# Performance work log

Hardware: AMD Instinct MI355X
Metric: run time of the kernel (lower is better)

Reference implementation:

```python
import jax, jax.numpy as jnp
import numpy as np

K = 9          # kernel_size
PAD = 4        # padding
N_OUT, C_IN = 32, 32


def setup_inputs() -> dict:
    key = jax.random.key(0)
    k1, k2, k3, k4, k5 = jax.random.split(key, 5)
    x = jax.random.normal(k1, (16, C_IN, 192, 192), jnp.float32)
    sx = jax.random.uniform(k2, (N_OUT, C_IN), jnp.float32, 0.2, 4.0)
    sy = jax.random.uniform(k3, (N_OUT, C_IN), jnp.float32, 0.2, 4.0)
    th = jax.random.uniform(k4, (N_OUT, C_IN), jnp.float32, 0.0, 2.0 * np.pi)
    weight = jnp.stack([sx, sy, th], axis=-1)          # [N, C, 3]
    bias = jax.random.normal(k5, (N_OUT,), jnp.float32) * 0.01
    return {"x": x, "weight": weight, "bias": bias}


def _gaussian_kernels(weight, k):
    # weight: [N, C, 3] -> normalized anisotropic Gaussian kernels [N, C, k, k]
    sx, sy = weight[..., 0], weight[..., 1]
    rad = weight[..., 2] / 180.0 * jnp.pi          # matches theta/180*pi in source
    c, s = jnp.cos(rad), jnp.sin(rad)
    sx2, sy2 = sx * sx, sy * sy
    # Sigma = U diag(sx^2, sy^2) U^T, U = [[c,-s],[s,c]] -> Sigma = [[a,b],[b,d]]
    a = c * c * sx2 + s * s * sy2
    b = c * s * (sx2 - sy2)
    d = s * s * sx2 + c * c * sy2
    det = a * d - b * b
    ia, ib, id_ = d / det, -b / det, a / det       # closed-form 2x2 inverse
    ax = jnp.arange(k, dtype=jnp.float32) - k // 2
    xx = ax[None, :]                               # x varies along columns
    yy = ax[:, None]                               # y varies along rows
    # quadratic form: ia*x^2 + 2*ib*x*y + id*y^2, broadcast to [N, C, k, k]
    q = (ia[..., None, None] * (xx * xx)
         + 2.0 * ib[..., None, None] * (xx * yy)
         + id_[..., None, None] * (yy * yy))
    ker = jnp.exp(-0.5 * q)
    return ker / jnp.sum(ker, axis=(-2, -1), keepdims=True)


def reference(x, weight, bias):
    w = _gaussian_kernels(weight, K)               # [N, C, K, K]
    out = jax.lax.conv_general_dilated(
        x, w, window_strides=(1, 1), padding=[(PAD, PAD), (PAD, PAD)],
        dimension_numbers=("NCHW", "OIHW", "NCHW"))
    return out + bias[None, :, None, None]
```

## Files before the change

kernel.cpp:

```cpp
#include <hip/hip_runtime.h>
#include <stdint.h>

#define H 192
#define W 192
#define CIN 32
#define NOUT 32
#define NB 16
#define PADI 4
#define HP 200
#define WP 200

#define HT 16
#define WTL 16
#define RROWS 24
#define RCOLS 24

typedef __attribute__((ext_vector_type(8))) short bf16x8;
typedef __attribute__((ext_vector_type(4))) float f32x4;

__device__ __forceinline__ unsigned short f2bf(float f) {
    union { float f; unsigned int u; } v; v.f = f;
    unsigned int r = v.u + 0x7fffu + ((v.u >> 16) & 1u);
    return (unsigned short)(r >> 16);
}

__device__ __forceinline__ void gload_lds16(const void* g, void* l) {
    __builtin_amdgcn_global_load_lds(
        (const __attribute__((address_space(1))) void*)g,
        (__attribute__((address_space(3))) void*)l, 16, 0, 0);
}

__global__ void genw_kernel(const float* __restrict__ wp, unsigned short* __restrict__ W2g) {
    const int b = blockIdx.x;
    const int o = b >> 5;
    const int i = b & 31;
    const int t = threadIdx.x;

    float sx = wp[b * 3 + 0], sy = wp[b * 3 + 1], th = wp[b * 3 + 2];
    float rad = th / 180.0f * 3.14159265358979323846f;
    float co = cosf(rad), si = sinf(rad);
    float sx2 = sx * sx, sy2 = sy * sy;
    float a = co * co * sx2 + si * si * sy2;
    float bb = co * si * (sx2 - sy2);
    float d = si * si * sx2 + co * co * sy2;
    float det = a * d - bb * bb;
    float ia = d / det, ib = -bb / det, idd = a / det;

    const int tap = t;
    float e = 0.0f;
    if (tap < 81) {
        float xx = (float)(tap % 9 - 4);
        float yy = (float)(tap / 9 - 4);
        float q = ia * xx * xx + 2.0f * ib * xx * yy + idd * yy * yy;
        e = expf(-0.5f * q);
    }
    float s = e;
    #pragma unroll
    for (int off = 32; off > 0; off >>= 1) s += __shfl_down(s, off);
    __shared__ float ws[2];
    if ((t & 63) == 0) ws[t >> 6] = s;
    __syncthreads();
    float total = ws[0] + ws[1];

    if (tap < 81) {
        int mt = o >> 4, m = o & 15, quad = i >> 3, j = i & 7;
        W2g[((((mt * 81 + tap) * 4 + quad) * 16 + m) << 3) + j] = f2bf(e / total);
    }
}

__global__ __launch_bounds__(256) void xpad_kernel(
    const float* __restrict__ x, unsigned short* __restrict__ xb)
{
    const int gid = blockIdx.x * 256 + threadIdx.x;
    const int wp4 = gid % (WP / 4);
    int rest = gid / (WP / 4);
    const int rp = rest % HP;
    rest /= HP;
    const int quad = rest & 3;
    const int n = rest >> 2;

    const int row = rp - PADI;
    const int col0 = wp4 * 4 - PADI;

    unsigned int d[4][4];
    #pragma unroll
    for (int p = 0; p < 4; p++)
        #pragma unroll
        for (int j = 0; j < 4; j++) d[p][j] = 0u;

    if ((unsigned)row < (unsigned)H && col0 >= 0 && col0 <= W - 4) {
        const float* p0 = x + (((size_t)(n * CIN + quad * 8)) * H + row) * (size_t)W + col0;
        #pragma unroll
        for (int k = 0; k < 8; ++k) {
            float4 v = *(const float4*)(p0 + (size_t)k * H * W);
            const int j = k >> 1;
            const int sh = (k & 1) * 16;
            d[0][j] |= (unsigned int)f2bf(v.x) << sh;
            d[1][j] |= (unsigned int)f2bf(v.y) << sh;
            d[2][j] |= (unsigned int)f2bf(v.z) << sh;
            d[3][j] |= (unsigned int)f2bf(v.w) << sh;
        }
    }
    unsigned short* dst = xb + (size_t)gid * 32;
    #pragma unroll
    for (int p = 0; p < 4; p++)
        *(uint4*)(dst + p * 8) = make_uint4(d[p][0], d[p][1], d[p][2], d[p][3]);
}

__global__ __launch_bounds__(512, 6) void conv_kernel(
    const unsigned short* __restrict__ xb, const unsigned short* __restrict__ W2g,
    const float* __restrict__ bias, float* __restrict__ out)
{
    __shared__ __align__(16) unsigned short ldsx[4 * RROWS * RCOLS * 8];

    const int t = threadIdx.x;
    const int bid = (blockIdx.x & 7) * 288 + (blockIdx.x >> 3);
    const int wb = bid % (W / WTL);
    const int hb = (bid / (W / WTL)) % (H / HT);
    const int n  = bid / ((W / WTL) * (H / HT));
    const int r0p = hb * HT;
    const int c0p = wb * WTL;
    const unsigned short* xbn = xb + (size_t)n * 4 * HP * WP * 8;

    #pragma unroll
    for (int it = 0; it < 4; ++it) {
        const int idx = it * 512 + t;
        const int w = idx % RCOLS;
        const int r = (idx / RCOLS) % RROWS;
        const int quad = idx / (RCOLS * RROWS);
        const size_t goff = (((size_t)(quad * HP + r0p + r)) * WP + (c0p + w)) * 8;
        gload_lds16(xbn + goff, &ldsx[(size_t)idx * 8]);
    }
    if (t < 256) {
        const int idx = 2048 + t;
        const int w = idx % RCOLS;
        const int r = (idx / RCOLS) % RROWS;
        const int quad = idx / (RCOLS * RROWS);
        const size_t goff = (((size_t)(quad * HP + r0p + r)) * WP + (c0p + w)) * 8;
        gload_lds16(xbn + goff, &ldsx[(size_t)idx * 8]);
    }

    const int wave = t >> 6;
    const int lane = t & 63;
    const int l15 = lane & 15;
    const int quad4 = lane >> 4;
    const int mt = wave & 1;
    const int rbase = (wave >> 1) * 4;

    const bf16x8* __restrict__ wbase =
        (const bf16x8*)W2g + (mt * 81 * 64 + quad4 * 16 + l15);

    bf16x8 A[9];
    #pragma unroll
    for (int dy = 0; dy < 9; dy++)
        A[dy] = wbase[(dy * 9 + 0) * 64];

    __syncthreads();

    f32x4 acc[4];
    #pragma unroll
    for (int i = 0; i < 4; i++) acc[i] = (f32x4){0.f, 0.f, 0.f, 0.f};

    const unsigned short* bptr = &ldsx[(size_t)(((quad4 * RROWS + rbase) * RCOLS) + l15) * 8];

    for (int dx = 0; dx < 9; dx++) {
        if (dx) {
            #pragma unroll
            for (int dy = 0; dy < 9; dy++)
                A[dy] = wbase[(dy * 9 + dx) * 64];
        }
        __builtin_amdgcn_s_setprio(1);
        bf16x8 bcur = *(const bf16x8*)&bptr[(size_t)(0 * RCOLS + dx) * 8];
        #pragma unroll
        for (int rr = 0; rr < 12; rr++) {
            const bf16x8 bnxt = (rr < 11)
                ? *(const bf16x8*)&bptr[(size_t)((rr + 1) * RCOLS + dx) * 8]
                : bcur;
            #pragma unroll
            for (int dy = 0; dy < 9; dy++) {
                const int orr = rr - dy;
                if (orr >= 0 && orr < 4) {
                    acc[orr] = __builtin_amdgcn_mfma_f32_16x16x32_bf16(
                        A[dy], bcur, acc[orr], 0, 0, 0);
                }
            }
            bcur = bnxt;
        }
        __builtin_amdgcn_s_setprio(0);
    }

    float* outn = out + (size_t)n * NOUT * H * W;
    float bb[4];
    #pragma unroll
    for (int reg = 0; reg < 4; reg++) bb[reg] = bias[mt * 16 + quad4 * 4 + reg];
    #pragma unroll
    for (int orr = 0; orr < 4; orr++) {
        const int row = hb * HT + rbase + orr;
        const int col = wb * WTL + l15;
        #pragma unroll
        for (int reg = 0; reg < 4; reg++) {
            const int och = mt * 16 + quad4 * 4 + reg;
            outn[((size_t)och * H + row) * W + col] = acc[orr][reg] + bb[reg];
        }
    }
}

__global__ __launch_bounds__(256, 4) void conv_kernel_legacy(
    const float* __restrict__ x, const unsigned short* __restrict__ W2g,
    const float* __restrict__ bias, float* __restrict__ out)
{
    __shared__ __align__(16) unsigned short ldsx[4 * RROWS * RCOLS * 8];

    const int t = threadIdx.x;
    const int bid = (blockIdx.x & 7) * 288 + (blockIdx.x >> 3);
    const int wb = bid % (W / WTL);
    const int hb = (bid / (W / WTL)) % (H / HT);
    const int n  = bid / ((W / WTL) * (H / HT));
    const int row0 = hb * HT - PADI;
    const int col0 = wb * WTL - PADI;
    const float* xn = x + (size_t)n * CIN * H * W;

    float v[9][8];
    #pragma unroll
    for (int it = 0; it < 9; ++it) {
        int idx = it * 256 + t;
        int w = idx % RCOLS;
        int r = (idx / RCOLS) % RROWS;
        int quad = idx / (RCOLS * RROWS);
        int row = row0 + r, col = col0 + w;
        #pragma unroll
        for (int k = 0; k < 8; k++) v[it][k] = 0.0f;
        if ((unsigned)row < (unsigned)H && (unsigned)col < (unsigned)W) {
            const float* p = xn + ((size_t)(quad * 8) * H + row) * W + col;
            #pragma unroll
            for (int k = 0; k < 8; k++) v[it][k] = p[(size_t)k * H * W];
        }
    }
    #pragma unroll
    for (int it = 0; it < 9; ++it) {
        int idx = it * 256 + t;
        unsigned int d[4];
        #pragma unroll
        for (int k = 0; k < 4; k++)
            d[k] = (unsigned int)f2bf(v[it][2 * k]) | ((unsigned int)f2bf(v[it][2 * k + 1]) << 16);
        *(uint4*)&ldsx[(size_t)idx * 8] = make_uint4(d[0], d[1], d[2], d[3]);
    }

    const int wave = t >> 6;
    const int lane = t & 63;
    const int l15 = lane & 15;
    const int quad4 = lane >> 4;
    const int mt = wave & 1;
    const int rbase = (wave >> 1) * 8;

    const bf16x8* __restrict__ Wpt = (const bf16x8*)W2g;

    bf16x8 A[2][9];
    #pragma unroll
    for (int dy = 0; dy < 9; dy++)
        A[0][dy] = Wpt[((mt * 81 + dy * 9 + 0) * 4 + quad4) * 16 + l15];

    __syncthreads();

    f32x4 acc[8];
    #pragma unroll
    for (int i = 0; i < 8; i++) acc[i] = (f32x4){0.f, 0.f, 0.f, 0.f};

    const unsigned short* bptr = &ldsx[(size_t)(((quad4 * RROWS + rbase) * RCOLS) + l15) * 8];

    #pragma unroll
    for (int dx = 0; dx < 9; dx++) {
        const int cur = dx & 1, nxt = cur ^ 1;
        if (dx < 8) {
            #pragma unroll
            for (int dy = 0; dy < 9; dy++)
                A[nxt][dy] = Wpt[((mt * 81 + dy * 9 + (dx + 1)) * 4 + quad4) * 16 + l15];
        }
        #pragma unroll
        for (int rr = 0; rr < 16; rr++) {
            const bf16x8 bfrag = *(const bf16x8*)&bptr[(size_t)(rr * RCOLS + dx) * 8];
            #pragma unroll
            for (int dy = 0; dy < 9; dy++) {
                const int orr = rr - dy;
                if (orr >= 0 && orr < 8) {
                    acc[orr] = __builtin_amdgcn_mfma_f32_16x16x32_bf16(
                        A[cur][dy], bfrag, acc[orr], 0, 0, 0);
                }
            }
        }
    }

    float* outn = out + (size_t)n * NOUT * H * W;
    float bb[4];
    #pragma unroll
    for (int reg = 0; reg < 4; reg++) bb[reg] = bias[mt * 16 + quad4 * 4 + reg];
    #pragma unroll
    for (int orr = 0; orr < 8; orr++) {
        const int row = hb * HT + rbase + orr;
        const int col = wb * WTL + l15;
        #pragma unroll
        for (int reg = 0; reg < 4; reg++) {
            const int och = mt * 16 + quad4 * 4 + reg;
            outn[((size_t)och * H + row) * W + col] = acc[orr][reg] + bb[reg];
        }
    }
}

extern "C" void kernel_launch(void* const* d_in, const int* in_sizes, int n_in,
                              void* d_out, int out_size, void* d_ws, size_t ws_size,
                              hipStream_t stream) {
    const float* x    = (const float*)d_in[0];
    const float* wp   = (const float*)d_in[1];
    const float* bias = (const float*)d_in[2];
    float* out = (float*)d_out;

    unsigned short* W2g = (unsigned short*)d_ws;
    const size_t XB_OFF = 262144;
    const size_t XB_BYTES = (size_t)NB * 4 * HP * WP * 8 * 2;
    unsigned short* xb = (unsigned short*)((char*)d_ws + XB_OFF);

    genw_kernel<<<NOUT * CIN, 128, 0, stream>>>(wp, W2g);

    const int blocks = NB * (H / HT) * (W / WTL);

    if (ws_size >= XB_OFF + XB_BYTES) {
        const int xpad_blocks = (NB * 4 * HP * (WP / 4)) / 256;
        xpad_kernel<<<xpad_blocks, 256, 0, stream>>>(x, xb);
        conv_kernel<<<blocks, 512, 0, stream>>>(xb, W2g, bias, out);
    } else {
        conv_kernel_legacy<<<blocks, 256, 0, stream>>>(x, W2g, bias, out);
    }
}
```

Measured before the change: 226.0 us.

## Make conv persistent with atomic tile scheduler and double-buffered LDS prefetch

Merges the weight-generation and pad/convert kernels into one prep launch, which removes a kernel launch. The conv kernel becomes persistent: 512 blocks of 256 threads pull tiles from an atomic counter. Each block prefetches the next tile's input into a second LDS buffer while computing the current one. Each wave now covers 8 output rows instead of 4, so every B fragment loaded from LDS feeds more MFMAs, and the weights are double-buffered in registers. In exchange, register and LDS pressure rise, occupancy drops (launch_bounds 256,2), and the kernel now relies on the counter being reset to zero in the prep kernel.

```diff
diff --git a/kernel.cpp b/kernel.cpp
--- a/kernel.cpp
+++ b/kernel.cpp
@@ -15,6 +15,10 @@
 #define RROWS 24
 #define RCOLS 24
 
+#define NT 2304
+#define BUFS (4 * RROWS * RCOLS * 8)
+#define XPAD_BLOCKS 2500
+
 typedef __attribute__((ext_vector_type(8))) short bf16x8;
 typedef __attribute__((ext_vector_type(4))) float f32x4;
 
@@ -30,11 +34,54 @@
         (__attribute__((address_space(3))) void*)l, 16, 0, 0);
 }
 
-__global__ void genw_kernel(const float* __restrict__ wp, unsigned short* __restrict__ W2g) {
-    const int b = blockIdx.x;
+__global__ __launch_bounds__(256) void prep_kernel(
+    const float* __restrict__ x, const float* __restrict__ wp,
+    unsigned short* __restrict__ xb, unsigned short* __restrict__ W2g,
+    int* __restrict__ cnt)
+{
+    const int t = threadIdx.x;
+    if (blockIdx.x < XPAD_BLOCKS) {
+        const int gid = blockIdx.x * 256 + t;
+        const int wp4 = gid % (WP / 4);
+        int rest = gid / (WP / 4);
+        const int rp = rest % HP;
+        rest /= HP;
+        const int quad = rest & 3;
+        const int n = rest >> 2;
+
+        const int row = rp - PADI;
+        const int col0 = wp4 * 4 - PADI;
+
+        unsigned int d[4][4];
+        #pragma unroll
+        for (int p = 0; p < 4; p++)
+            #pragma unroll
+            for (int j = 0; j < 4; j++) d[p][j] = 0u;
+
+        if ((unsigned)row < (unsigned)H && col0 >= 0 && col0 <= W - 4) {
+            const float* p0 = x + (((size_t)(n * CIN + quad * 8)) * H + row) * (size_t)W + col0;
+            #pragma unroll
+            for (int k = 0; k < 8; ++k) {
+                float4 v = *(const float4*)(p0 + (size_t)k * H * W);
+                const int j = k >> 1;
+                const int sh = (k & 1) * 16;
+                d[0][j] |= (unsigned int)f2bf(v.x) << sh;
+                d[1][j] |= (unsigned int)f2bf(v.y) << sh;
+                d[2][j] |= (unsigned int)f2bf(v.z) << sh;
+                d[3][j] |= (unsigned int)f2bf(v.w) << sh;
+            }
+        }
+        unsigned short* dst = xb + (size_t)gid * 32;
+        #pragma unroll
+        for (int p = 0; p < 4; p++)
+            *(uint4*)(dst + p * 8) = make_uint4(d[p][0], d[p][1], d[p][2], d[p][3]);
+        return;
+    }
+
+    const int b = blockIdx.x - XPAD_BLOCKS;
+    if (b == 0 && t == 0) *cnt = 0;
     const int o = b >> 5;
     const int i = b & 31;
-    const int t = threadIdx.x;
 
     float sx = wp[b * 3 + 0], sy = wp[b * 3 + 1], th = wp[b * 3 + 2];
     float rad = th / 180.0f * 3.14159265358979323846f;
@@ -57,10 +104,10 @@
     float s = e;
     #pragma unroll
     for (int off = 32; off > 0; off >>= 1) s += __shfl_down(s, off);
-    __shared__ float ws[2];
+    __shared__ float ws[4];
     if ((t & 63) == 0) ws[t >> 6] = s;
     __syncthreads();
-    float total = ws[0] + ws[1];
+    float total = ws[0] + ws[1] + ws[2] + ws[3];
 
     if (tap < 81) {
         int mt = o >> 4, m = o & 15, quad = i >> 3, j = i & 7;
@@ -68,140 +115,168 @@
     }
 }
 
-__global__ __launch_bounds__(256) void xpad_kernel(
-    const float* __restrict__ x, unsigned short* __restrict__ xb)
+__global__ __launch_bounds__(256, 2) void conv_kernel(
+    const unsigned short* __restrict__ xb, const unsigned short* __restrict__ W2g,
+    const float* __restrict__ bias, float* __restrict__ out, int* __restrict__ cnt)
 {
-    const int gid = blockIdx.x * 256 + threadIdx.x;
-    const int wp4 = gid % (WP / 4);
-    int rest = gid / (WP / 4);
-    const int rp = rest % HP;
-    rest /= HP;
-    const int quad = rest & 3;
-    const int n = rest >> 2;
-
-    const int row = rp - PADI;
-    const int col0 = wp4 * 4 - PADI;
-
-    unsigned int d[4][4];
-    #pragma unroll
-    for (int p = 0; p < 4; p++)
-        #pragma unroll
-        for (int j = 0; j < 4; j++) d[p][j] = 0u;
-
-    if ((unsigned)row < (unsigned)H && col0 >= 0 && col0 <= W - 4) {
-        const float* p0 = x + (((size_t)(n * CIN + quad * 8)) * H + row) * (size_t)W + col0;
-        #pragma unroll
-        for (int k = 0; k < 8; ++k) {
-            float4 v = *(const float4*)(p0 + (size_t)k * H * W);
-            const int j = k >> 1;
-            const int sh = (k & 1) * 16;
-            d[0][j] |= (unsigned int)f2bf(v.x) << sh;
-            d[1][j] |= (unsigned int)f2bf(v.y) << sh;
-            d[2][j] |= (unsigned int)f2bf(v.z) << sh;
-            d[3][j] |= (unsigned int)f2bf(v.w) << sh;
-        }
-    }
-    unsigned short* dst = xb + (size_t)gid * 32;
-    #pragma unroll
-    for (int p = 0; p < 4; p++)
-        *(uint4*)(dst + p * 8) = make_uint4(d[p][0], d[p][1], d[p][2], d[p][3]);
-}
-
-__global__ __launch_bounds__(512, 6) void conv_kernel(
-    const unsigned short* __restrict__ xb, const unsigned short* __restrict__ W2g,
-    const float* __restrict__ bias, float* __restrict__ out)
-{
-    __shared__ __align__(16) unsigned short ldsx[4 * RROWS * RCOLS * 8];
+    __shared__ __align__(16) unsigned short ldsx[2 * BUFS];
+    __shared__ int sg[2];
 
     const int t = threadIdx.x;
-    const int bid = (blockIdx.x & 7) * 288 + (blockIdx.x >> 3);
-    const int wb = bid % (W / WTL);
-    const int hb = (bid / (W / WTL)) % (H / HT);
-    const int n  = bid / ((W / WTL) * (H / HT));
-    const int r0p = hb * HT;
-    const int c0p = wb * WTL;
-    const unsigned short* xbn = xb + (size_t)n * 4 * HP * WP * 8;
-
-    #pragma unroll
-    for (int it = 0; it < 4; ++it) {
-        const int idx = it * 512 + t;
-        const int w = idx % RCOLS;
-        const int r = (idx / RCOLS) % RROWS;
-        const int quad = idx / (RCOLS * RROWS);
-        const size_t goff = (((size_t)(quad * HP + r0p + r)) * WP + (c0p + w)) * 8;
-        gload_lds16(xbn + goff, &ldsx[(size_t)idx * 8]);
-    }
-    if (t < 256) {
-        const int idx = 2048 + t;
-        const int w = idx % RCOLS;
-        const int r = (idx / RCOLS) % RROWS;
-        const int quad = idx / (RCOLS * RROWS);
-        const size_t goff = (((size_t)(quad * HP + r0p + r)) * WP + (c0p + w)) * 8;
-        gload_lds16(xbn + goff, &ldsx[(size_t)idx * 8]);
-    }
-
     const int wave = t >> 6;
     const int lane = t & 63;
     const int l15 = lane & 15;
     const int quad4 = lane >> 4;
     const int mt = wave & 1;
-    const int rbase = (wave >> 1) * 4;
-
-    const bf16x8* __restrict__ wbase =
-        (const bf16x8*)W2g + (mt * 81 * 64 + quad4 * 16 + l15);
-
-    bf16x8 A[9];
-    #pragma unroll
-    for (int dy = 0; dy < 9; dy++)
-        A[dy] = wbase[(dy * 9 + 0) * 64];
-
+    const int rbase = (wave >> 1) * 8;
+
+    const bf16x8* __restrict__ Wpt = (const bf16x8*)W2g;
+
+    float bb[4];
+    #pragma unroll
+    for (int reg = 0; reg < 4; reg++) bb[reg] = bias[mt * 16 + quad4 * 4 + reg];
+
+    if (t == 0) sg[0] = atomicAdd(cnt, 1);
     __syncthreads();
-
-    f32x4 acc[4];
-    #pragma unroll
-    for (int i = 0; i < 4; i++) acc[i] = (f32x4){0.f, 0.f, 0.f, 0.f};
-
-    const unsigned short* bptr = &ldsx[(size_t)(((quad4 * RROWS + rbase) * RCOLS) + l15) * 8];
-
-    for (int dx = 0; dx < 9; dx++) {
-        if (dx) {
-            #pragma unroll
-            for (int dy = 0; dy < 9; dy++)
-                A[dy] = wbase[(dy * 9 + dx) * 64];
-        }
-        __builtin_amdgcn_s_setprio(1);
-        bf16x8 bcur = *(const bf16x8*)&bptr[(size_t)(0 * RCOLS + dx) * 8];
-        #pragma unroll
-        for (int rr = 0; rr < 12; rr++) {
-            const bf16x8 bnxt = (rr < 11)
-                ? *(const bf16x8*)&bptr[(size_t)((rr + 1) * RCOLS + dx) * 8]
-                : bcur;
-            #pragma unroll
-            for (int dy = 0; dy < 9; dy++) {
-                const int orr = rr - dy;
-                if (orr >= 0 && orr < 4) {
-                    acc[orr] = __builtin_amdgcn_mfma_f32_16x16x32_bf16(
-                        A[dy], bcur, acc[orr], 0, 0, 0);
+    int g = sg[0];
+
+    {
+        const int wb = g % (W / WTL);
+        const int hb = (g / (W / WTL)) % (H / HT);
+        const int n  = g / ((W / WTL) * (H / HT));
+        const unsigned short* xbn = xb + (size_t)n * 4 * HP * WP * 8;
+        const int r0p = hb * HT, c0p = wb * WTL;
+        #pragma unroll
+        for (int it = 0; it < 9; ++it) {
+            const int idx = it * 256 + t;
+            const int w = idx % RCOLS;
+            const int r = (idx / RCOLS) % RROWS;
+            const int quad = idx / (RCOLS * RROWS);
+            const size_t goff = (((size_t)(quad * HP + r0p + r)) * WP + (c0p + w)) * 8;
+            gload_lds16(xbn + goff, &ldsx[(size_t)idx * 8]);
+        }
+    }
+    if (t == 0) sg[1] = atomicAdd(cnt, 1);
+
+    __syncthreads();
+
+    int p = 1, cur = 0;
+    while (true) {
+        const int gn = sg[p];
+        const bool more = (gn < NT);
+        if (more) {
+            const int wb = gn % (W / WTL);
+            const int hb = (gn / (W / WTL)) % (H / HT);
+            const int n  = gn / ((W / WTL) * (H / HT));
+            const unsigned short* xbn = xb + (size_t)n * 4 * HP * WP * 8;
+            const int r0p = hb * HT, c0p = wb * WTL;
+            const int bufo = (cur ^ 1) * BUFS;
+            #pragma unroll
+            for (int it = 0; it < 9; ++it) {
+                const int idx = it * 256 + t;
+                const int w = idx % RCOLS;
+                const int r = (idx / RCOLS) % RROWS;
+                const int quad = idx / (RCOLS * RROWS);
+                const size_t goff = (((size_t)(quad * HP + r0p + r)) * WP + (c0p + w)) * 8;
+                gload_lds16(xbn + goff, &ldsx[(size_t)(bufo + idx * 8)]);
+            }
+            if (t == 0) sg[p ^ 1] = atomicAdd(cnt, 1);
+        }
+
+        bf16x8 A[2][9];
+        #pragma unroll
+        for (int dy = 0; dy < 9; dy++)
+            A[0][dy] = Wpt[((mt * 81 + dy * 9 + 0) * 4 + quad4) * 16 + l15];
+
+        f32x4 acc[8];
+        #pragma unroll
+        for (int i = 0; i < 8; i++) acc[i] = (f32x4){0.f, 0.f, 0.f, 0.f};
+
+        const unsigned short* bptr =
+            &ldsx[cur * BUFS + (size_t)(((quad4 * RROWS + rbase) * RCOLS) + l15) * 8];
+
+        #pragma unroll
+        for (int dx = 0; dx < 9; dx++) {
+            const int cu = dx & 1, nx = cu ^ 1;
+            if (dx < 8) {
+                #pragma unroll
+                for (int dy = 0; dy < 9; dy++)
+                    A[nx][dy] = Wpt[((mt * 81 + dy * 9 + (dx + 1)) * 4 + quad4) * 16 + l15];
+            }
+            __builtin_amdgcn_s_setprio(1);
+            #pragma unroll
+            for (int rr = 0; rr < 16; rr++) {
+                const bf16x8 bfrag = *(const bf16x8*)&bptr[(size_t)(rr * RCOLS + dx) * 8];
+                #pragma unroll
+                for (int dy = 0; dy < 9; dy++) {
+                    const int orr = rr - dy;
+                    if (orr >= 0 && orr < 8) {
+                        acc[orr] = __builtin_amdgcn_mfma_f32_16x16x32_bf16(
+                            A[cu][dy], bfrag, acc[orr], 0, 0, 0);
+                    }
                 }
             }
-            bcur = bnxt;
-        }
-        __builtin_amdgcn_s_setprio(0);
-    }
-
-    float* outn = out + (size_t)n * NOUT * H * W;
-    float bb[4];
-    #pragma unroll
-    for (int reg = 0; reg < 4; reg++) bb[reg] = bias[mt * 16 + quad4 * 4 + reg];
-    #pragma unroll
-    for (int orr = 0; orr < 4; orr++) {
-        const int row = hb * HT + rbase + orr;
-        const int col = wb * WTL + l15;
-        #pragma unroll
-        for (int reg = 0; reg < 4; reg++) {
-            const int och = mt * 16 + quad4 * 4 + reg;
-            outn[((size_t)och * H + row) * W + col] = acc[orr][reg] + bb[reg];
-        }
+            __builtin_amdgcn_s_setprio(0);
+        }
+
+        {
+            const int wb = g % (W / WTL);
+            const int hb = (g / (W / WTL)) % (H / HT);
+            const int n  = g / ((W / WTL) * (H / HT));
+            float* outn = out + (size_t)n * NOUT * H * W;
+            #pragma unroll
+            for (int orr = 0; orr < 8; orr++) {
+                const int row = hb * HT + rbase + orr;
+                const int col = wb * WTL + l15;
+                #pragma unroll
+                for (int reg = 0; reg < 4; reg++) {
+                    const int och = mt * 16 + quad4 * 4 + reg;
+                    outn[((size_t)och * H + row) * W + col] = acc[orr][reg] + bb[reg];
+                }
+            }
+        }
+
+        if (!more) break;
+        __syncthreads();
+        g = gn; p ^= 1; cur ^= 1;
+    }
+}
+
+__global__ void genw_kernel(const float* __restrict__ wp, unsigned short* __restrict__ W2g) {
+    const int b = blockIdx.x;
+    const int o = b >> 5;
+    const int i = b & 31;
+    const int t = threadIdx.x;
+
+    float sx = wp[b * 3 + 0], sy = wp[b * 3 + 1], th = wp[b * 3 + 2];
+    float rad = th / 180.0f * 3.14159265358979323846f;
+    float co = cosf(rad), si = sinf(rad);
+    float sx2 = sx * sx, sy2 = sy * sy;
+    float a = co * co * sx2 + si * si * sy2;
+    float bb = co * si * (sx2 - sy2);
+    float d = si * si * sx2 + co * co * sy2;
+    float det = a * d - bb * bb;
+    float ia = d / det, ib = -bb / det, idd = a / det;
+
+    const int tap = t;
+    float e = 0.0f;
+    if (tap < 81) {
+        float xx = (float)(tap % 9 - 4);
+        float yy = (float)(tap / 9 - 4);
+        float q = ia * xx * xx + 2.0f * ib * xx * yy + idd * yy * yy;
+        e = expf(-0.5f * q);
+    }
+    float s = e;
+    #pragma unroll
+    for (int off = 32; off > 0; off >>= 1) s += __shfl_down(s, off);
+    __shared__ float ws[2];
+    if ((t & 63) == 0) ws[t >> 6] = s;
+    __syncthreads();
+    float total = ws[0] + ws[1];
+
+    if (tap < 81) {
+        int mt = o >> 4, m = o & 15, quad = i >> 3, j = i & 7;
+        W2g[((((mt * 81 + tap) * 4 + quad) * 16 + m) << 3) + j] = f2bf(e / total);
     }
 }
 
@@ -315,19 +390,18 @@
     float* out = (float*)d_out;
 
     unsigned short* W2g = (unsigned short*)d_ws;
-    const size_t XB_OFF = 262144;
+    const size_t CNT_OFF = 196608;
+    const size_t XB_OFF  = 262144;
     const size_t XB_BYTES = (size_t)NB * 4 * HP * WP * 8 * 2;
+    int* cnt = (int*)((char*)d_ws + CNT_OFF);
     unsigned short* xb = (unsigned short*)((char*)d_ws + XB_OFF);
 
-    genw_kernel<<<NOUT * CIN, 128, 0, stream>>>(wp, W2g);
-
-    const int blocks = NB * (H / HT) * (W / WTL);
-
     if (ws_size >= XB_OFF + XB_BYTES) {
-        const int xpad_blocks = (NB * 4 * HP * (WP / 4)) / 256;
-        xpad_kernel<<<xpad_blocks, 256, 0, stream>>>(x, xb);
-        conv_kernel<<<blocks, 512, 0, stream>>>(xb, W2g, bias, out);
+        prep_kernel<<<XPAD_BLOCKS + NOUT * CIN, 256, 0, stream>>>(x, wp, xb, W2g, cnt);
+        conv_kernel<<<512, 256, 0, stream>>>(xb, W2g, bias, out, cnt);
     } else {
+        genw_kernel<<<NOUT * CIN, 128, 0, stream>>>(wp, W2g);
+        const int blocks = NB * (H / HT) * (W / WTL);
         conv_kernel_legacy<<<blocks, 256, 0, stream>>>(x, W2g, bias, out);
     }
 }
```

New measurement: 269.7 us. +19.4%, slower.
